# Kernel tuning notes

Hardware: AMD Instinct MI355X
Metric: run time of the kernel (lower is better)

Reference implementation:

```python
import jax, jax.numpy as jnp
import numpy as np

VOCAB = 50000
D = 512          # in_feat == word_embedding_dim
B = 4096
S = 128
NUM_LABELS = 3


def setup_inputs() -> dict:
    key = jax.random.key(0)
    ks = jax.random.split(key, 16)
    ids_a = jax.random.randint(ks[0], (B, S), 0, VOCAB, dtype=jnp.int32)
    ids_b = jax.random.randint(ks[1], (B, S), 0, VOCAB, dtype=jnp.int32)
    mask_a = jax.random.randint(ks[2], (B, S), 0, 2) > 0
    mask_b = jax.random.randint(ks[3], (B, S), 0, 2) > 0
    s = 0.02
    W_emb = jax.random.normal(ks[4], (VOCAB, D), jnp.float32) * s
    W_emb = W_emb.at[0].set(0.0)  # padding_idx=0
    enc_w1 = jax.random.normal(ks[5], (D, D), jnp.float32) * s
    enc_b1 = jnp.zeros((D,), jnp.float32)
    enc_w2 = jax.random.normal(ks[6], (D, D), jnp.float32) * s
    enc_b2 = jnp.zeros((D,), jnp.float32)
    cls_w1 = jax.random.normal(ks[7], (2 * D, D), jnp.float32) * s
    cls_b1 = jnp.zeros((D,), jnp.float32)
    cls_w2 = jax.random.normal(ks[8], (D, NUM_LABELS), jnp.float32) * s
    cls_b2 = jnp.zeros((NUM_LABELS,), jnp.float32)
    return {
        "text_a_inputs_id": ids_a, "text_b_inputs_id": ids_b,
        "text_a_attention_mask": mask_a, "text_b_attention_mask": mask_b,
        "W_emb": W_emb,
        "enc_w1": enc_w1, "enc_b1": enc_b1, "enc_w2": enc_w2, "enc_b2": enc_b2,
        "cls_w1": cls_w1, "cls_b1": cls_b1, "cls_w2": cls_w2, "cls_b2": cls_b2,
    }


def _encode(ids, mask, W_emb, w1, b1, w2, b2):
    # embedding gather [B,S,D], fused masked sum-pool -> [B,D]
    emb = W_emb[ids]
    pooled = jnp.einsum("bsd,bs->bd", emb, mask.astype(emb.dtype))
    x = jnp.tanh(pooled @ w1 + b1)
    x = jnp.tanh(x @ w2 + b2)  # dropout is identity in eval
    return x


def reference(text_a_inputs_id, text_b_inputs_id, text_a_attention_mask,
              text_b_attention_mask, W_emb, enc_w1, enc_b1, enc_w2, enc_b2,
              cls_w1, cls_b1, cls_w2, cls_b2):
    va = _encode(text_a_inputs_id, text_a_attention_mask, W_emb, enc_w1, enc_b1, enc_w2, enc_b2)
    vb = _encode(text_b_inputs_id, text_b_attention_mask, W_emb, enc_w1, enc_b1, enc_w2, enc_b2)
    pooled = jnp.concatenate([va, vb], axis=-1)  # [B, 2D]
    h = jnp.tanh(pooled @ cls_w1 + cls_b1)
    logits = h @ cls_w2 + cls_b2  # [B, num_labels]
    return logits
```

## Files before the change

kernel.cpp:

```cpp
#include <hip/hip_runtime.h>


typedef unsigned short u16;
typedef __attribute__((ext_vector_type(8))) short short8;
typedef __attribute__((ext_vector_type(4))) float f32x4;

__device__ __forceinline__ float bfu2f(u16 u) {
    union { unsigned int i; float f; } v;
    v.i = ((unsigned int)u) << 16;
    return v.f;
}

__device__ __forceinline__ u16 f2bfu(float f) {
    union { float f; unsigned int i; } v;
    v.f = f;
    unsigned int x = v.i;
    x += 0x7fffu + ((x >> 16) & 1u);
    return (u16)(x >> 16);
}

__device__ __forceinline__ float fast_tanh(float x) {
    float xc = fminf(fmaxf(x, -15.f), 15.f);
    float e = __builtin_amdgcn_exp2f(xc * 2.885390082f);
    return (e - 1.f) / (e + 1.f);
}

__device__ __forceinline__ int detect_wave(const u16* __restrict__ W,
                                           const unsigned int* __restrict__ m,
                                           int lane)
{
    int cnt = 0;
    int w01 = 1, b01 = 1, lo16 = 0;
    #pragma unroll
    for (int j = lane; j < 256; j += 64) {
        u16 u = W[1024 + 2 * j];
        int e = (u >> 7) & 0xFF;
        cnt += (e >= 0x6A && e <= 0x7E) ? 1 : 0;
        unsigned int v = m[j];
        w01 &= (v <= 1u) ? 1 : 0;
        b01 &= ((v & ~0x01010101u) == 0u) ? 1 : 0;
        lo16 |= ((v & 0xFFFFu) == 0x3F80u) ? 1 : 0;
    }
    #pragma unroll
    for (int off = 32; off > 0; off >>= 1) {
        cnt  += __shfl_down(cnt, off);
        w01  &= __shfl_down(w01, off);
        b01  &= __shfl_down(b01, off);
        lo16 |= __shfl_down(lo16, off);
    }
    int mtype;
    if (w01)        mtype = 0;
    else if (b01)   mtype = 1;
    else if (lo16)  mtype = 2;
    else            mtype = 3;
    int fl = ((cnt >= 128) ? 1 : 0) | (mtype << 2);
    return __shfl(fl, 0);
}

__device__ __forceinline__ int mask_nonzero(const void* __restrict__ msk,
                                            int idx, int mtype)
{
    switch (mtype) {
        case 0:  return ((const int*)msk)[idx] != 0;
        case 1:  return ((const unsigned char*)msk)[idx] != 0;
        case 2:  return ((const u16*)msk)[idx] != 0;
        default: return ((const unsigned int*)msk)[idx] != 0u;
    }
}

__global__ __launch_bounds__(128) void pool_kernel(
    const int* __restrict__ ids_a, const int* __restrict__ ids_b,
    const void* __restrict__ mska, const void* __restrict__ mskb,
    const void* __restrict__ W, u16* __restrict__ P,
    const unsigned int* __restrict__ Mdet)
{
    __shared__ int s_ids[128];
    __shared__ int s_cnt;
    __shared__ int s_flags;
    __shared__ float sP[512];
    const int t = threadIdx.x;
    const int w = t >> 6;
    const int lane = t & 63;

    if (t == 0) s_cnt = 0;
    if (t < 64) {
        int fl = detect_wave((const u16*)W, Mdet, t);
        if (t == 0) s_flags = fl;
    }
    __syncthreads();
    const int  flags = s_flags;
    const bool isbf  = (flags & 1) != 0;
    const int  mtype = (flags >> 2) & 3;

    const int row = blockIdx.x;
    const int r   = row & 4095;
    const int* __restrict__ ids = (row < 4096) ? ids_a : ids_b;
    const void* __restrict__ msk = (row < 4096) ? mska : mskb;

    int id = ids[r * 128 + t];
    int mk = mask_nonzero(msk, r * 128 + t, mtype);
    if (mk) {
        int idx = atomicAdd(&s_cnt, 1);
        s_ids[idx] = id;
    }
    __syncthreads();
    const int cnt = s_cnt;

    float acc[8] = {};
    if (isbf) {
        const u16* Wb = (const u16*)W;
        int j = w;
        for (; j + 6 < cnt; j += 8) {
            union { uint4 v; u16 s[8]; } r0, r1, r2, r3;
            r0.v = *(const uint4*)(Wb + (size_t)s_ids[j + 0] * 512 + lane * 8);
            r1.v = *(const uint4*)(Wb + (size_t)s_ids[j + 2] * 512 + lane * 8);
            r2.v = *(const uint4*)(Wb + (size_t)s_ids[j + 4] * 512 + lane * 8);
            r3.v = *(const uint4*)(Wb + (size_t)s_ids[j + 6] * 512 + lane * 8);
            #pragma unroll
            for (int i = 0; i < 8; ++i)
                acc[i] += bfu2f(r0.s[i]) + bfu2f(r1.s[i]) +
                          bfu2f(r2.s[i]) + bfu2f(r3.s[i]);
        }
        for (; j < cnt; j += 2) {
            union { uint4 v; u16 s[8]; } rr;
            rr.v = *(const uint4*)(Wb + (size_t)s_ids[j] * 512 + lane * 8);
            #pragma unroll
            for (int i = 0; i < 8; ++i) acc[i] += bfu2f(rr.s[i]);
        }
    } else {
        const float* Wf = (const float*)W;
        for (int j = w; j < cnt; j += 2) {
            const float* rp = Wf + (size_t)s_ids[j] * 512 + lane * 8;
            float4 a = *(const float4*)(rp + 0);
            float4 b = *(const float4*)(rp + 4);
            acc[0] += a.x; acc[1] += a.y; acc[2] += a.z; acc[3] += a.w;
            acc[4] += b.x; acc[5] += b.y; acc[6] += b.z; acc[7] += b.w;
        }
    }

    if (w == 0) {
        #pragma unroll
        for (int i = 0; i < 8; ++i) sP[lane * 8 + i] = acc[i];
    }
    __syncthreads();
    if (w == 1) {
        union { uint4 v; u16 s[8]; } o;
        #pragma unroll
        for (int i = 0; i < 8; ++i)
            o.s[i] = f2bfu(acc[i] + sP[lane * 8 + i]);
        *(uint4*)(P + (size_t)row * 512 + lane * 8) = o.v;
    }
}

template<bool ISBF>
__device__ __forceinline__ void enc12_body(
    u16* __restrict__ P,
    const void* __restrict__ w1v, const void* __restrict__ b1v,
    const void* __restrict__ w2v, const void* __restrict__ b2v,
    u16* __restrict__ Bs, u16* __restrict__ Xbuf)
{
    const int tid  = threadIdx.x;
    const int lane = tid & 63;
    const int wid  = tid >> 6;
    const int wm   = (wid & 1) * 16;
    const int wn   = (wid >> 1) * 16;
    const int lm   = lane & 15;
    const int kq   = lane >> 4;
    const int kc   = kq * 8;
    const int R0   = blockIdx.x * 32;

    const int bk = tid >> 3;
    const int jn = tid & 7;
    const int nb = jn * 8;

    const u16*   b1b = (const u16*)b1v; const float* b1f = (const float*)b1v;
    const u16*   b2b = (const u16*)b2v; const float* b2f = (const float*)b2v;

    short8 af[16];
    {
        const u16* arow = P + (size_t)(R0 + wm + lm) * 512 + kc;
        #pragma unroll
        for (int s = 0; s < 16; ++s)
            af[s] = *(const short8*)(arow + s * 32);
    }
    short8 af2[16];

    const u16* Wb; const float* Wf;
    uint4 rb0, rb1;
    float4 rf00, rf01, rf10, rf11;

#define FETCHW(k0, n0)                                                        \
    {                                                                         \
        const int kr0 = (k0) + bk;                                            \
        const int kr1 = (k0) + bk + 64;                                       \
        if constexpr (ISBF) {                                                 \
            rb0 = *(const uint4*)(Wb + (size_t)kr0 * 512 + (n0) + nb);        \
            rb1 = *(const uint4*)(Wb + (size_t)kr1 * 512 + (n0) + nb);        \
        } else {                                                              \
            const float* p0_ = Wf + (size_t)kr0 * 512 + (n0) + nb;            \
            const float* p1_ = Wf + (size_t)kr1 * 512 + (n0) + nb;            \
            rf00 = *(const float4*)p0_; rf01 = *(const float4*)(p0_ + 4);     \
            rf10 = *(const float4*)p1_; rf11 = *(const float4*)(p1_ + 4);     \
        }                                                                     \
    }

#define STOREW(pp)                                                            \
    {                                                                         \
        u16 bv0[8], bv1[8];                                                   \
        if constexpr (ISBF) {                                                 \
            union { uint4 v; u16 s[8]; } u0_, u1_;                            \
            u0_.v = rb0; u1_.v = rb1;                                         \
            _Pragma("unroll")                                                 \
            for (int i = 0; i < 8; ++i) { bv0[i] = u0_.s[i]; bv1[i] = u1_.s[i]; } \
        } else {                                                              \
            bv0[0]=f2bfu(rf00.x); bv0[1]=f2bfu(rf00.y);                       \
            bv0[2]=f2bfu(rf00.z); bv0[3]=f2bfu(rf00.w);                       \
            bv0[4]=f2bfu(rf01.x); bv0[5]=f2bfu(rf01.y);                       \
            bv0[6]=f2bfu(rf01.z); bv0[7]=f2bfu(rf01.w);                       \
            bv1[0]=f2bfu(rf10.x); bv1[1]=f2bfu(rf10.y);                       \
            bv1[2]=f2bfu(rf10.z); bv1[3]=f2bfu(rf10.w);                       \
            bv1[4]=f2bfu(rf11.x); bv1[5]=f2bfu(rf11.y);                       \
            bv1[6]=f2bfu(rf11.z); bv1[7]=f2bfu(rf11.w);                       \
        }                                                                     \
        const int o0_ = ((((bk >> 3) + jn) & 15)) * 8 + (bk & 7);             \
        const int o1_ = ((((bk >> 3) + 8 + jn) & 15)) * 8 + (bk & 7);         \
        _Pragma("unroll")                                                     \
        for (int i = 0; i < 8; ++i) {                                         \
            Bs[(pp) * 8704 + (nb + i) * 136 + o0_] = bv0[i];                  \
            Bs[(pp) * 8704 + (nb + i) * 136 + o1_] = bv1[i];                  \
        }                                                                     \
    }

#define KLOOP(afin)                                                           \
    FETCHW(0, n0) STOREW(0) FETCHW(128, n0)                                   \
    __syncthreads();                                                          \
    _Pragma("unroll")                                                         \
    for (int kb = 0; kb < 4; ++kb) {                                          \
        const int p_ = kb & 1;                                                \
        if (kb < 3) { STOREW(p_ ^ 1) if (kb < 2) FETCHW((kb + 2) * 128, n0) } \
        _Pragma("unroll")                                                     \
        for (int s = 0; s < 4; ++s) {                                         \
            const int n_ = wn + lm;                                           \
            const int ch = (((s * 4 + kq) + (n_ >> 3)) & 15) * 8;             \
            short8 bf = *(const short8*)&Bs[p_ * 8704 + n_ * 136 + ch];       \
            acc = __builtin_amdgcn_mfma_f32_16x16x32_bf16(afin[kb * 4 + s],   \
                                                          bf, acc, 0, 0, 0);  \
        }                                                                     \
        if (kb < 3) __syncthreads();                                          \
    }

    Wb = (const u16*)w1v; Wf = (const float*)w1v;
    #pragma unroll
    for (int t = 0; t < 8; ++t) {
        const int n0 = t * 64;
        f32x4 acc = (f32x4){0.f, 0.f, 0.f, 0.f};
        KLOOP(af)
        const int   ncol = n0 + wn + lm;
        const float bia  = ISBF ? bfu2f(b1b[ncol]) : b1f[ncol];
        u16* xw = Xbuf + (t & 1) * (32 * 72);
        #pragma unroll
        for (int r = 0; r < 4; ++r)
            xw[(wm + kq * 4 + r) * 72 + wn + lm] =
                f2bfu(fast_tanh(acc[r] + bia));
        __syncthreads();
        const u16* xr = Xbuf + (t & 1) * (32 * 72) + (size_t)(wm + lm) * 72;
        af2[2 * t + 0] = *(const short8*)(xr + kc);
        af2[2 * t + 1] = *(const short8*)(xr + 32 + kc);
    }

    Wb = (const u16*)w2v; Wf = (const float*)w2v;
    #pragma unroll 1
    for (int t2 = 0; t2 < 8; ++t2) {
        const int n0 = t2 * 64;
        f32x4 acc = (f32x4){0.f, 0.f, 0.f, 0.f};
        KLOOP(af2)
        const int   ncol = n0 + wn + lm;
        const float bia  = ISBF ? bfu2f(b2b[ncol]) : b2f[ncol];
        #pragma unroll
        for (int r = 0; r < 4; ++r)
            P[(size_t)(R0 + wm + kq * 4 + r) * 512 + ncol] =
                f2bfu(fast_tanh(acc[r] + bia));
        __syncthreads();
    }
#undef KLOOP
#undef STOREW
#undef FETCHW
}

__global__ __launch_bounds__(512, 2) void enc12_kernel(
    u16* __restrict__ P,
    const void* __restrict__ w1, const void* __restrict__ b1,
    const void* __restrict__ w2, const void* __restrict__ b2,
    const u16* __restrict__ Wdet, const unsigned int* __restrict__ Mdet)
{
    __shared__ __align__(16) u16 Bs[2 * 8704];
    __shared__ __align__(16) u16 Xbuf[2 * 32 * 72];
    __shared__ int s_flags;

    if (threadIdx.x < 64) {
        int fl = detect_wave(Wdet, Mdet, threadIdx.x);
        if (threadIdx.x == 0) s_flags = fl;
    }
    __syncthreads();
    if (s_flags & 1) enc12_body<true >(P, w1, b1, w2, b2, Bs, Xbuf);
    else             enc12_body<false>(P, w1, b1, w2, b2, Bs, Xbuf);
}

template<bool ISBF>
__device__ __forceinline__ void g3_body(
    const u16* __restrict__ A, const u16* __restrict__ A2, const int K1,
    const void* __restrict__ Bv, const void* __restrict__ biasv,
    const void* __restrict__ w2v, const void* __restrict__ cb2v,
    float* __restrict__ outp, const int K,
    u16* __restrict__ As0, u16* __restrict__ Bs0)
{
    const int tid  = threadIdx.x;
    const int lane = tid & 63;
    const int wid = tid >> 6;
    const int wm  = (wid & 3) * 32;
    const int wn  = (wid >> 2) * 32;
    const int ar = tid >> 2;
    const int ak = (tid & 3) * 8;
    const int bk = tid >> 3;
    const int jn = tid & 7;
    const int nb = jn * 8;
    const int bofs = (((bk >> 3) + jn) & 3) * 8 + (bk & 7);
    const int lm = lane & 15;
    const int kq = lane >> 4;
    const int kc = kq * 8;
    const int m0 = (blockIdx.x & 31) * 128;
    const int n0 = (blockIdx.x >> 5) * 64;

    const u16*   Bb = (const u16*)Bv;
    const float* Bf = (const float*)Bv;

    f32x4 acc[2][2];
    #pragma unroll
    for (int i = 0; i < 2; ++i)
        #pragma unroll
        for (int j = 0; j < 2; ++j)
            acc[i][j] = (f32x4){0.f, 0.f, 0.f, 0.f};

    uint4 ra, rbb;
    float4 rf0, rf1;

#define FETCH(k0)                                                             \
    {                                                                         \
        const int kg = (k0) + ak;                                             \
        const u16* base = (kg < K1) ? (A + kg) : (A2 + (kg - K1));            \
        ra = *(const uint4*)(base + (size_t)(m0 + ar) * 512);                 \
        if (tid < 256) {                                                      \
            if constexpr (ISBF) {                                             \
                rbb = *(const uint4*)(Bb + (size_t)((k0) + bk) * 512 + n0 + nb);\
            } else {                                                          \
                const float* Bp = Bf + (size_t)((k0) + bk) * 512 + n0 + nb;   \
                rf0 = *(const float4*)(Bp + 0);                               \
                rf1 = *(const float4*)(Bp + 4);                               \
            }                                                                 \
        }                                                                     \
    }

#define STORE(pp)                                                             \
    {                                                                         \
        *(uint4*)&As0[(pp) * 5120 + ar * 40 + ak] = ra;                       \
        if (tid < 256) {                                                      \
            u16 bvals[8];                                                     \
            if constexpr (ISBF) {                                             \
                union { uint4 v; u16 s[8]; } ub; ub.v = rbb;                  \
                _Pragma("unroll")                                             \
                for (int i = 0; i < 8; ++i) bvals[i] = ub.s[i];               \
            } else {                                                          \
                bvals[0] = f2bfu(rf0.x); bvals[1] = f2bfu(rf0.y);             \
                bvals[2] = f2bfu(rf0.z); bvals[3] = f2bfu(rf0.w);             \
                bvals[4] = f2bfu(rf1.x); bvals[5] = f2bfu(rf1.y);             \
                bvals[6] = f2bfu(rf1.z); bvals[7] = f2bfu(rf1.w);             \
            }                                                                 \
            _Pragma("unroll")                                                 \
            for (int i = 0; i < 8; ++i)                                       \
                Bs0[(pp) * 2560 + (nb + i) * 40 + bofs] = bvals[i];           \
        }                                                                     \
    }

    FETCH(0)
    STORE(0)
    FETCH(32)
    __syncthreads();

    int p = 0;
    for (int k0 = 0; k0 < K; k0 += 32) {
        if (k0 + 32 < K) {
            STORE(p ^ 1)
            if (k0 + 64 < K) FETCH(k0 + 64)
        }
        const u16* Ap = As0 + p * 5120;
        const u16* Bp2 = Bs0 + p * 2560;
        short8 afr[2], bfr[2];
        #pragma unroll
        for (int i = 0; i < 2; ++i)
            afr[i] = *(const short8*)&Ap[(wm + i * 16 + lm) * 40 + kc];
        #pragma unroll
        for (int j = 0; j < 2; ++j) {
            const int n = wn + j * 16 + lm;
            const int ch = ((kq + (n >> 3)) & 3) * 8;
            bfr[j] = *(const short8*)&Bp2[n * 40 + ch];
        }
        #pragma unroll
        for (int i = 0; i < 2; ++i)
            #pragma unroll
            for (int j = 0; j < 2; ++j)
                acc[i][j] = __builtin_amdgcn_mfma_f32_16x16x32_bf16(
                    afr[i], bfr[j], acc[i][j], 0, 0, 0);
        if (k0 + 32 < K) __syncthreads();
        p ^= 1;
    }
#undef FETCH
#undef STORE

    float lg[2][4][3];
    #pragma unroll
    for (int i = 0; i < 2; ++i)
        #pragma unroll
        for (int r = 0; r < 4; ++r)
            #pragma unroll
            for (int l = 0; l < 3; ++l) lg[i][r][l] = 0.f;

    #pragma unroll
    for (int j = 0; j < 2; ++j) {
        const int n = n0 + wn + j * 16 + lm;
        const float bsv = ISBF ? bfu2f(((const u16*)biasv)[n])
                               : ((const float*)biasv)[n];
        float wc[3];
        #pragma unroll
        for (int l = 0; l < 3; ++l)
            wc[l] = ISBF ? bfu2f(((const u16*)w2v)[n * 3 + l])
                         : ((const float*)w2v)[n * 3 + l];
        #pragma unroll
        for (int i = 0; i < 2; ++i)
            #pragma unroll
            for (int r = 0; r < 4; ++r) {
                const float h = fast_tanh(acc[i][j][r] + bsv);
                #pragma unroll
                for (int l = 0; l < 3; ++l) lg[i][r][l] += h * wc[l];
            }
    }
    #pragma unroll
    for (int off = 1; off <= 8; off <<= 1)
        #pragma unroll
        for (int i = 0; i < 2; ++i)
            #pragma unroll
            for (int r = 0; r < 4; ++r)
                #pragma unroll
                for (int l = 0; l < 3; ++l)
                    lg[i][r][l] += __shfl_xor(lg[i][r][l], off);

    if (lm == 0) {
        const bool addb = (n0 == 0) && (wn == 0);
        float cb[3];
        #pragma unroll
        for (int l = 0; l < 3; ++l)
            cb[l] = ISBF ? bfu2f(((const u16*)cb2v)[l])
                         : ((const float*)cb2v)[l];
        #pragma unroll
        for (int i = 0; i < 2; ++i)
            #pragma unroll
            for (int r = 0; r < 4; ++r) {
                const int m = m0 + wm + i * 16 + kq * 4 + r;
                #pragma unroll
                for (int l = 0; l < 3; ++l) {
                    float v = lg[i][r][l];
                    if (addb) v += cb[l];
                    atomicAdd(&outp[m * 3 + l], v);
                }
            }
    }
}

__global__ __launch_bounds__(512, 2) void gemm3_logits(
    const u16* __restrict__ A, const u16* __restrict__ A2, int K1,
    const void* __restrict__ B, const void* __restrict__ bias,
    const void* __restrict__ w2, const void* __restrict__ cb2,
    float* __restrict__ out, int K,
    const u16* __restrict__ Wdet, const unsigned int* __restrict__ Mdet)
{
    __shared__ __align__(16) u16 As[2 * 128 * 40];
    __shared__ __align__(16) u16 Bs[2 * 64 * 40];
    __shared__ int s_flags;

    if (threadIdx.x < 64) {
        int fl = detect_wave(Wdet, Mdet, threadIdx.x);
        if (threadIdx.x == 0) s_flags = fl;
    }
    __syncthreads();
    if (s_flags & 1)
        g3_body<true >(A, A2, K1, B, bias, w2, cb2, out, K, As, Bs);
    else
        g3_body<false>(A, A2, K1, B, bias, w2, cb2, out, K, As, Bs);
}

extern "C" void kernel_launch(void* const* d_in, const int* in_sizes, int n_in,
                              void* d_out, int out_size, void* d_ws, size_t ws_size,
                              hipStream_t stream)
{
    const int* ids_a  = (const int*)d_in[0];
    const int* ids_b  = (const int*)d_in[1];
    const void* mask_a = d_in[2];
    const void* mask_b = d_in[3];
    const void* W_emb  = d_in[4];
    const void* enc_w1 = d_in[5];
    const void* enc_b1 = d_in[6];
    const void* enc_w2 = d_in[7];
    const void* enc_b2 = d_in[8];
    const void* cls_w1 = d_in[9];
    const void* cls_b1 = d_in[10];
    const void* cls_w2 = d_in[11];
    const void* cls_b2 = d_in[12];

    const u16* Wdet = (const u16*)W_emb;
    const unsigned int* Mdet = (const unsigned int*)mask_a;

    u16* buf0 = (u16*)d_ws;
    float* outp = (float*)d_out;

    hipMemsetAsync(d_out, 0, 4096 * 3 * sizeof(float), stream);

    pool_kernel<<<8192, 128, 0, stream>>>(ids_a, ids_b, mask_a, mask_b,
                                          W_emb, buf0, Mdet);

    enc12_kernel<<<256, 512, 0, stream>>>(buf0, enc_w1, enc_b1,
                                          enc_w2, enc_b2, Wdet, Mdet);

    gemm3_logits<<<256, 512, 0, stream>>>(
        buf0, buf0 + (size_t)4096 * 512, 512, cls_w1, cls_b1,
        cls_w2, cls_b2, outp, 1024, Wdet, Mdet);
}
```

Measured before the change: 409.5 us.

## Restructure encoder MLP kernel to gather weights directly from global memory, 16-row tiles

The two-layer encoder kernel no longer stages weight tiles through double-buffered shared memory. Each wave now gathers its B fragments with strided scalar loads straight from global (L2-cached) weights and computes 64 output columns for a 16-row tile, and the grid doubles to 512 blocks. This removes the LDS staging and most barriers and is meant to raise parallelism. In exchange it issues many uncoalesced 2- or 4-byte global loads and converts fp32 weights to bf16 repeatedly, with less weight reuse per block.

```diff
diff --git a/kernel.cpp b/kernel.cpp
--- a/kernel.cpp
+++ b/kernel.cpp
@@ -157,134 +157,103 @@
     u16* __restrict__ P,
     const void* __restrict__ w1v, const void* __restrict__ b1v,
     const void* __restrict__ w2v, const void* __restrict__ b2v,
-    u16* __restrict__ Bs, u16* __restrict__ Xbuf)
+    u16* __restrict__ Xbuf)
 {
     const int tid  = threadIdx.x;
     const int lane = tid & 63;
     const int wid  = tid >> 6;
-    const int wm   = (wid & 1) * 16;
-    const int wn   = (wid >> 1) * 16;
+    const int wn64 = wid * 64;
     const int lm   = lane & 15;
     const int kq   = lane >> 4;
-    const int kc   = kq * 8;
-    const int R0   = blockIdx.x * 32;
-
-    const int bk = tid >> 3;
-    const int jn = tid & 7;
-    const int nb = jn * 8;
+    const int R0   = blockIdx.x * 16;
 
     const u16*   b1b = (const u16*)b1v; const float* b1f = (const float*)b1v;
     const u16*   b2b = (const u16*)b2v; const float* b2f = (const float*)b2v;
 
-    short8 af[16];
+#define GATHB(dst, Wb_, Wf_, kbase, col)                                      \
+    {                                                                         \
+        union { short8 v; u16 s[8]; } u_;                                     \
+        if constexpr (ISBF) {                                                 \
+            const u16* bp_ = (Wb_) + (size_t)(kbase) * 512 + (col);           \
+            _Pragma("unroll")                                                 \
+            for (int j_ = 0; j_ < 8; ++j_) u_.s[j_] = bp_[j_ * 512];          \
+        } else {                                                              \
+            const float* fp_ = (Wf_) + (size_t)(kbase) * 512 + (col);         \
+            _Pragma("unroll")                                                 \
+            for (int j_ = 0; j_ < 8; ++j_) u_.s[j_] = f2bfu(fp_[j_ * 512]);   \
+        }                                                                     \
+        dst = u_.v;                                                           \
+    }
+
+    const u16*   W1b = (const u16*)w1v;  const float* W1f = (const float*)w1v;
+    f32x4 acc0 = (f32x4){0.f,0.f,0.f,0.f};
+    f32x4 acc1 = (f32x4){0.f,0.f,0.f,0.f};
+    f32x4 acc2 = (f32x4){0.f,0.f,0.f,0.f};
+    f32x4 acc3 = (f32x4){0.f,0.f,0.f,0.f};
+    #pragma unroll 4
+    for (int kb = 0; kb < 16; ++kb) {
+        const int k0 = kb * 32 + kq * 8;
+        short8 a = *(const short8*)(P + (size_t)(R0 + lm) * 512 + k0);
+        short8 b0, b1_, b2_, b3;
+        GATHB(b0, W1b, W1f, k0, wn64 + 0  + lm)
+        GATHB(b1_, W1b, W1f, k0, wn64 + 16 + lm)
+        GATHB(b2_, W1b, W1f, k0, wn64 + 32 + lm)
+        GATHB(b3, W1b, W1f, k0, wn64 + 48 + lm)
+        acc0 = __builtin_amdgcn_mfma_f32_16x16x32_bf16(a, b0, acc0, 0, 0, 0);
+        acc1 = __builtin_amdgcn_mfma_f32_16x16x32_bf16(a, b1_, acc1, 0, 0, 0);
+        acc2 = __builtin_amdgcn_mfma_f32_16x16x32_bf16(a, b2_, acc2, 0, 0, 0);
+        acc3 = __builtin_amdgcn_mfma_f32_16x16x32_bf16(a, b3, acc3, 0, 0, 0);
+    }
     {
-        const u16* arow = P + (size_t)(R0 + wm + lm) * 512 + kc;
-        #pragma unroll
-        for (int s = 0; s < 16; ++s)
-            af[s] = *(const short8*)(arow + s * 32);
-    }
+        f32x4* accs[4] = { &acc0, &acc1, &acc2, &acc3 };
+        #pragma unroll
+        for (int sub = 0; sub < 4; ++sub) {
+            const int col = wn64 + sub * 16 + lm;
+            const float bia = ISBF ? bfu2f(b1b[col]) : b1f[col];
+            #pragma unroll
+            for (int r = 0; r < 4; ++r)
+                Xbuf[(kq * 4 + r) * 520 + col] =
+                    f2bfu(fast_tanh((*accs[sub])[r] + bia));
+        }
+    }
+    __syncthreads();
+
     short8 af2[16];
-
-    const u16* Wb; const float* Wf;
-    uint4 rb0, rb1;
-    float4 rf00, rf01, rf10, rf11;
-
-#define FETCHW(k0, n0)                                                        \
-    {                                                                         \
-        const int kr0 = (k0) + bk;                                            \
-        const int kr1 = (k0) + bk + 64;                                       \
-        if constexpr (ISBF) {                                                 \
-            rb0 = *(const uint4*)(Wb + (size_t)kr0 * 512 + (n0) + nb);        \
-            rb1 = *(const uint4*)(Wb + (size_t)kr1 * 512 + (n0) + nb);        \
-        } else {                                                              \
-            const float* p0_ = Wf + (size_t)kr0 * 512 + (n0) + nb;            \
-            const float* p1_ = Wf + (size_t)kr1 * 512 + (n0) + nb;            \
-            rf00 = *(const float4*)p0_; rf01 = *(const float4*)(p0_ + 4);     \
-            rf10 = *(const float4*)p1_; rf11 = *(const float4*)(p1_ + 4);     \
-        }                                                                     \
-    }
-
-#define STOREW(pp)                                                            \
-    {                                                                         \
-        u16 bv0[8], bv1[8];                                                   \
-        if constexpr (ISBF) {                                                 \
-            union { uint4 v; u16 s[8]; } u0_, u1_;                            \
-            u0_.v = rb0; u1_.v = rb1;                                         \
-            _Pragma("unroll")                                                 \
-            for (int i = 0; i < 8; ++i) { bv0[i] = u0_.s[i]; bv1[i] = u1_.s[i]; } \
-        } else {                                                              \
-            bv0[0]=f2bfu(rf00.x); bv0[1]=f2bfu(rf00.y);                       \
-            bv0[2]=f2bfu(rf00.z); bv0[3]=f2bfu(rf00.w);                       \
-            bv0[4]=f2bfu(rf01.x); bv0[5]=f2bfu(rf01.y);                       \
-            bv0[6]=f2bfu(rf01.z); bv0[7]=f2bfu(rf01.w);                       \
-            bv1[0]=f2bfu(rf10.x); bv1[1]=f2bfu(rf10.y);                       \
-            bv1[2]=f2bfu(rf10.z); bv1[3]=f2bfu(rf10.w);                       \
-            bv1[4]=f2bfu(rf11.x); bv1[5]=f2bfu(rf11.y);                       \
-            bv1[6]=f2bfu(rf11.z); bv1[7]=f2bfu(rf11.w);                       \
-        }                                                                     \
-        const int o0_ = ((((bk >> 3) + jn) & 15)) * 8 + (bk & 7);             \
-        const int o1_ = ((((bk >> 3) + 8 + jn) & 15)) * 8 + (bk & 7);         \
-        _Pragma("unroll")                                                     \
-        for (int i = 0; i < 8; ++i) {                                         \
-            Bs[(pp) * 8704 + (nb + i) * 136 + o0_] = bv0[i];                  \
-            Bs[(pp) * 8704 + (nb + i) * 136 + o1_] = bv1[i];                  \
-        }                                                                     \
-    }
-
-#define KLOOP(afin)                                                           \
-    FETCHW(0, n0) STOREW(0) FETCHW(128, n0)                                   \
-    __syncthreads();                                                          \
-    _Pragma("unroll")                                                         \
-    for (int kb = 0; kb < 4; ++kb) {                                          \
-        const int p_ = kb & 1;                                                \
-        if (kb < 3) { STOREW(p_ ^ 1) if (kb < 2) FETCHW((kb + 2) * 128, n0) } \
-        _Pragma("unroll")                                                     \
-        for (int s = 0; s < 4; ++s) {                                         \
-            const int n_ = wn + lm;                                           \
-            const int ch = (((s * 4 + kq) + (n_ >> 3)) & 15) * 8;             \
-            short8 bf = *(const short8*)&Bs[p_ * 8704 + n_ * 136 + ch];       \
-            acc = __builtin_amdgcn_mfma_f32_16x16x32_bf16(afin[kb * 4 + s],   \
-                                                          bf, acc, 0, 0, 0);  \
-        }                                                                     \
-        if (kb < 3) __syncthreads();                                          \
-    }
-
-    Wb = (const u16*)w1v; Wf = (const float*)w1v;
-    #pragma unroll
-    for (int t = 0; t < 8; ++t) {
-        const int n0 = t * 64;
-        f32x4 acc = (f32x4){0.f, 0.f, 0.f, 0.f};
-        KLOOP(af)
-        const int   ncol = n0 + wn + lm;
-        const float bia  = ISBF ? bfu2f(b1b[ncol]) : b1f[ncol];
-        u16* xw = Xbuf + (t & 1) * (32 * 72);
-        #pragma unroll
-        for (int r = 0; r < 4; ++r)
-            xw[(wm + kq * 4 + r) * 72 + wn + lm] =
-                f2bfu(fast_tanh(acc[r] + bia));
-        __syncthreads();
-        const u16* xr = Xbuf + (t & 1) * (32 * 72) + (size_t)(wm + lm) * 72;
-        af2[2 * t + 0] = *(const short8*)(xr + kc);
-        af2[2 * t + 1] = *(const short8*)(xr + 32 + kc);
-    }
-
-    Wb = (const u16*)w2v; Wf = (const float*)w2v;
-    #pragma unroll 1
-    for (int t2 = 0; t2 < 8; ++t2) {
-        const int n0 = t2 * 64;
-        f32x4 acc = (f32x4){0.f, 0.f, 0.f, 0.f};
-        KLOOP(af2)
-        const int   ncol = n0 + wn + lm;
-        const float bia  = ISBF ? bfu2f(b2b[ncol]) : b2f[ncol];
-        #pragma unroll
-        for (int r = 0; r < 4; ++r)
-            P[(size_t)(R0 + wm + kq * 4 + r) * 512 + ncol] =
-                f2bfu(fast_tanh(acc[r] + bia));
-        __syncthreads();
-    }
-#undef KLOOP
-#undef STOREW
-#undef FETCHW
+    #pragma unroll
+    for (int s = 0; s < 16; ++s)
+        af2[s] = *(const short8*)&Xbuf[lm * 520 + s * 32 + kq * 8];
+
+    const u16*   W2b = (const u16*)w2v;  const float* W2f = (const float*)w2v;
+    acc0 = (f32x4){0.f,0.f,0.f,0.f};
+    acc1 = (f32x4){0.f,0.f,0.f,0.f};
+    acc2 = (f32x4){0.f,0.f,0.f,0.f};
+    acc3 = (f32x4){0.f,0.f,0.f,0.f};
+    #pragma unroll 4
+    for (int kb = 0; kb < 16; ++kb) {
+        const int k0 = kb * 32 + kq * 8;
+        short8 b0, b1_, b2_, b3;
+        GATHB(b0, W2b, W2f, k0, wn64 + 0  + lm)
+        GATHB(b1_, W2b, W2f, k0, wn64 + 16 + lm)
+        GATHB(b2_, W2b, W2f, k0, wn64 + 32 + lm)
+        GATHB(b3, W2b, W2f, k0, wn64 + 48 + lm)
+        acc0 = __builtin_amdgcn_mfma_f32_16x16x32_bf16(af2[kb], b0, acc0, 0, 0, 0);
+        acc1 = __builtin_amdgcn_mfma_f32_16x16x32_bf16(af2[kb], b1_, acc1, 0, 0, 0);
+        acc2 = __builtin_amdgcn_mfma_f32_16x16x32_bf16(af2[kb], b2_, acc2, 0, 0, 0);
+        acc3 = __builtin_amdgcn_mfma_f32_16x16x32_bf16(af2[kb], b3, acc3, 0, 0, 0);
+    }
+    {
+        f32x4* accs[4] = { &acc0, &acc1, &acc2, &acc3 };
+        #pragma unroll
+        for (int sub = 0; sub < 4; ++sub) {
+            const int col = wn64 + sub * 16 + lm;
+            const float bia = ISBF ? bfu2f(b2b[col]) : b2f[col];
+            #pragma unroll
+            for (int r = 0; r < 4; ++r)
+                P[(size_t)(R0 + kq * 4 + r) * 512 + col] =
+                    f2bfu(fast_tanh((*accs[sub])[r] + bia));
+        }
+    }
+#undef GATHB
 }
 
 __global__ __launch_bounds__(512, 2) void enc12_kernel(
@@ -293,8 +262,7 @@
     const void* __restrict__ w2, const void* __restrict__ b2,
     const u16* __restrict__ Wdet, const unsigned int* __restrict__ Mdet)
 {
-    __shared__ __align__(16) u16 Bs[2 * 8704];
-    __shared__ __align__(16) u16 Xbuf[2 * 32 * 72];
+    __shared__ __align__(16) u16 Xbuf[16 * 520];
     __shared__ int s_flags;
 
     if (threadIdx.x < 64) {
@@ -302,8 +270,8 @@
         if (threadIdx.x == 0) s_flags = fl;
     }
     __syncthreads();
-    if (s_flags & 1) enc12_body<true >(P, w1, b1, w2, b2, Bs, Xbuf);
-    else             enc12_body<false>(P, w1, b1, w2, b2, Bs, Xbuf);
+    if (s_flags & 1) enc12_body<true >(P, w1, b1, w2, b2, Xbuf);
+    else             enc12_body<false>(P, w1, b1, w2, b2, Xbuf);
 }
 
 template<bool ISBF>
@@ -526,7 +494,7 @@
     pool_kernel<<<8192, 128, 0, stream>>>(ids_a, ids_b, mask_a, mask_b,
                                           W_emb, buf0, Mdet);
 
-    enc12_kernel<<<256, 512, 0, stream>>>(buf0, enc_w1, enc_b1,
+    enc12_kernel<<<512, 512, 0, stream>>>(buf0, enc_w1, enc_b1,
                                           enc_w2, enc_b2, Wdet, Mdet);
 
     gemm3_logits<<<256, 512, 0, stream>>>(
```

Result: slower. 431.4 us (+5.4%).
